# Kernel optimization log

Hardware: AMD Instinct MI355X
Metric: run time of the kernel (lower is better)

## Reference

```python
import jax, jax.numpy as jnp
import numpy as np

B, T, D, F, E = 4, 8192, 1024, 4096, 8


def setup_inputs() -> dict:
    key = jax.random.key(0)
    ks = jax.random.split(key, 5)
    s = 0.02
    return {
        "X": jax.random.normal(ks[0], (B, T, D), dtype=jnp.float32),
        "slots_w": jax.random.normal(ks[1], (E, D), dtype=jnp.float32) * s,
        "w1": jax.random.normal(ks[2], (E, F, D), dtype=jnp.float32) * s,
        "w3": jax.random.normal(ks[3], (E, F, D), dtype=jnp.float32) * s,
        "w2": jax.random.normal(ks[4], (E, D, F), dtype=jnp.float32) * s,
    }


def reference(X, slots_w, w1, w3, w2):
    # logits: [B,T,E]
    logits = jnp.einsum("btd,ed->bte", X, slots_w)
    dispatch_w = jax.nn.softmax(logits, axis=1)  # softmax over tokens
    combine_w = jax.nn.softmax(logits, axis=2)   # softmax over experts
    # slots: one D-vector per expert per batch -> [B,E,D]
    slots = jnp.einsum("bte,btd->bed", dispatch_w, X)
    # SwiGLU FFN batched over experts
    h = jax.nn.silu(jnp.einsum("bed,efd->bef", slots, w1)) * jnp.einsum("bed,efd->bef", slots, w3)
    y = jnp.einsum("bef,edf->bed", h, w2)  # [B,E,D]
    # combine back to tokens: [B,T,D]
    return jnp.einsum("bte,bed->btd", combine_w, y)
```

## Files before the change

### kernel.cpp

```cpp
#include <hip/hip_runtime.h>
#include <math.h>

#define NB 4
#define NT 8192
#define ND 1024
#define NF 4096
#define NE 8

#define K3_CHUNKS 128
#define K3_TPC (NT / K3_CHUNKS)
#define K7_CHB 256
#define K7_TOK (NT / K7_CHB)

typedef float v4f __attribute__((ext_vector_type(4)));

__device__ __forceinline__ float4 ntload4(const float* p) {
  v4f v = __builtin_nontemporal_load((const v4f*)p);
  return make_float4(v.x, v.y, v.z, v.w);
}
__device__ __forceinline__ void ntstore4(float* p, float4 a) {
  v4f v = {a.x, a.y, a.z, a.w};
  __builtin_nontemporal_store(v, (v4f*)p);
}

__device__ __forceinline__ float dot4(float4 a, float4 b) {
  return a.x * b.x + a.y * b.y + a.z * b.z + a.w * b.w;
}

__device__ __forceinline__ float reduce8(float v0, float v1, float v2, float v3,
                                         float v4, float v5, float v6, float v7,
                                         int lane) {
  const bool b0 = lane & 1;
  float s, u0, u1, u2, u3;
  s = b0 ? v0 : v1; u0 = (b0 ? v1 : v0) + __shfl_xor(s, 1);
  s = b0 ? v2 : v3; u1 = (b0 ? v3 : v2) + __shfl_xor(s, 1);
  s = b0 ? v4 : v5; u2 = (b0 ? v5 : v4) + __shfl_xor(s, 1);
  s = b0 ? v6 : v7; u3 = (b0 ? v7 : v6) + __shfl_xor(s, 1);
  const bool b1 = lane & 2;
  float w0, w1;
  s = b1 ? u0 : u1; w0 = (b1 ? u1 : u0) + __shfl_xor(s, 2);
  s = b1 ? u2 : u3; w1 = (b1 ? u3 : u2) + __shfl_xor(s, 2);
  const bool b2 = lane & 4;
  s = b2 ? w0 : w1; float x = (b2 ? w1 : w0) + __shfl_xor(s, 4);
  x += __shfl_xor(x, 8);
  x += __shfl_xor(x, 16);
  x += __shfl_xor(x, 32);
  return x;
}

__global__ __launch_bounds__(256, 4) void k_logits(const float* __restrict__ X,
                                                   const float* __restrict__ sw,
                                                   float* __restrict__ logits) {
  __shared__ float4 s_sw[NE * ND / 4];
  for (int i = threadIdx.x; i < NE * ND / 4; i += 256)
    s_sw[i] = ((const float4*)sw)[i];
  __syncthreads();
  const int lane = threadIdx.x & 63;
  const int wave = threadIdx.x >> 6;
  const int b = blockIdx.x >> 9;
  const int t0 = (blockIdx.x & 511) * 16;

  float4 Xc[4], Xn[4];
  {
    const float4* xr = (const float4*)(X + ((size_t)b * NT + t0 + wave) * ND);
#pragma unroll
    for (int it = 0; it < 4; ++it) Xc[it] = xr[it * 64 + lane];
  }
#pragma unroll
  for (int i = 0; i < 4; ++i) {
    const int t = t0 + wave + i * 4;
    if (i < 3) {
      const float4* xr = (const float4*)(X + ((size_t)b * NT + t + 4) * ND);
#pragma unroll
      for (int it = 0; it < 4; ++it) Xn[it] = xr[it * 64 + lane];
    }
    float acc[NE];
#pragma unroll
    for (int e = 0; e < NE; ++e) acc[e] = 0.f;
#pragma unroll
    for (int it = 0; it < 4; ++it) {
      float4 x = Xc[it];
#pragma unroll
      for (int e = 0; e < NE; ++e)
        acc[e] += dot4(x, s_sw[e * 256 + it * 64 + lane]);
    }
    float r = reduce8(acc[0], acc[1], acc[2], acc[3],
                      acc[4], acc[5], acc[6], acc[7], lane);
    if (lane < 8) logits[((size_t)b * NT + t) * NE + lane] = r;
#pragma unroll
    for (int it = 0; it < 4; ++it) Xc[it] = Xn[it];
  }
}

__global__ __launch_bounds__(256) void k_colstats(const float* __restrict__ logits,
                                                  float* __restrict__ M,
                                                  float* __restrict__ L) {
  const int b = blockIdx.x / NE;
  const int e = blockIdx.x % NE;
  const int tid = threadIdx.x;
  const int lane = tid & 63, wave = tid >> 6;
  const float* base = logits + (size_t)b * NT * NE + e;
  float v[NT / 256];
#pragma unroll
  for (int i = 0; i < NT / 256; ++i) v[i] = base[(size_t)(tid + i * 256) * NE];
  float mx = -1e30f;
#pragma unroll
  for (int i = 0; i < NT / 256; ++i) mx = fmaxf(mx, v[i]);
#pragma unroll
  for (int off = 32; off > 0; off >>= 1) mx = fmaxf(mx, __shfl_xor(mx, off));
  __shared__ float red[4];
  if (lane == 0) red[wave] = mx;
  __syncthreads();
  mx = fmaxf(fmaxf(red[0], red[1]), fmaxf(red[2], red[3]));
  float s = 0.f;
#pragma unroll
  for (int i = 0; i < NT / 256; ++i) s += expf(v[i] - mx);
#pragma unroll
  for (int off = 32; off > 0; off >>= 1) s += __shfl_xor(s, off);
  __syncthreads();
  if (lane == 0) red[wave] = s;
  __syncthreads();
  if (tid == 0) {
    M[blockIdx.x] = mx;
    L[blockIdx.x] = red[0] + red[1] + red[2] + red[3];
  }
}

__global__ __launch_bounds__(256, 2) void k_slots_partial(const float* __restrict__ X,
                                                          const float* __restrict__ logits,
                                                          const float* __restrict__ M,
                                                          float* __restrict__ partial) {
  __shared__ float pw[K3_TPC][NE];
  __shared__ float sM[NE];
  const int tid = threadIdx.x;
  const int b = blockIdx.x / K3_CHUNKS;
  const int chunk = blockIdx.x % K3_CHUNKS;
  const int t0 = chunk * K3_TPC;
  if (tid < NE) sM[tid] = M[b * NE + tid];
  __syncthreads();
  for (int i = tid; i < K3_TPC * NE; i += 256) {
    const int t = i >> 3, e = i & 7;
    pw[t][e] = expf(logits[((size_t)b * NT + t0 + t) * NE + e] - sM[e]);
  }
  __syncthreads();

  const float* xb = X + ((size_t)b * NT + t0) * ND + tid * 4;
  float4 Xc[8], Xn[8];
#pragma unroll
  for (int k = 0; k < 8; ++k) Xc[k] = *(const float4*)(xb + (size_t)k * ND);
  float4 acc[NE];
#pragma unroll
  for (int e = 0; e < NE; ++e) acc[e] = make_float4(0.f, 0.f, 0.f, 0.f);

  for (int g = 0; g < 8; ++g) {
    if (g < 7) {
#pragma unroll
      for (int k = 0; k < 8; ++k)
        Xn[k] = *(const float4*)(xb + (size_t)((g + 1) * 8 + k) * ND);
    }
#pragma unroll
    for (int k = 0; k < 8; ++k) {
      const int t = g * 8 + k;
      float4 pa = *(const float4*)&pw[t][0];
      float4 pb = *(const float4*)&pw[t][4];
      float4 x = Xc[k];
      acc[0].x += pa.x * x.x; acc[0].y += pa.x * x.y; acc[0].z += pa.x * x.z; acc[0].w += pa.x * x.w;
      acc[1].x += pa.y * x.x; acc[1].y += pa.y * x.y; acc[1].z += pa.y * x.z; acc[1].w += pa.y * x.w;
      acc[2].x += pa.z * x.x; acc[2].y += pa.z * x.y; acc[2].z += pa.z * x.z; acc[2].w += pa.z * x.w;
      acc[3].x += pa.w * x.x; acc[3].y += pa.w * x.y; acc[3].z += pa.w * x.z; acc[3].w += pa.w * x.w;
      acc[4].x += pb.x * x.x; acc[4].y += pb.x * x.y; acc[4].z += pb.x * x.z; acc[4].w += pb.x * x.w;
      acc[5].x += pb.y * x.x; acc[5].y += pb.y * x.y; acc[5].z += pb.y * x.z; acc[5].w += pb.y * x.w;
      acc[6].x += pb.z * x.x; acc[6].y += pb.z * x.y; acc[6].z += pb.z * x.z; acc[6].w += pb.z * x.w;
      acc[7].x += pb.w * x.x; acc[7].y += pb.w * x.y; acc[7].z += pb.w * x.z; acc[7].w += pb.w * x.w;
    }
#pragma unroll
    for (int k = 0; k < 8; ++k) Xc[k] = Xn[k];
  }
  float* pout = partial + (size_t)blockIdx.x * (NE * ND) + tid * 4;
#pragma unroll
  for (int e = 0; e < NE; ++e) *(float4*)(pout + e * ND) = acc[e];
}

__global__ __launch_bounds__(256, 4) void k_slots_reduce(const float* __restrict__ partial,
                                                         const float* __restrict__ L,
                                                         float* __restrict__ slots) {
  __shared__ float red[256];
  const int tid = threadIdx.x;
  const int half = tid >> 7;
  const int l128 = tid & 127;
  const int col = blockIdx.x * 128 + l128;
  const int b = col >> 13;
  const int ed = col & 8191;
  const float* p = partial + ((size_t)b * K3_CHUNKS + half * 64) * (NE * ND) + ed;
  float s = 0.f;
  for (int c = 0; c < 64; c += 8) {
#pragma unroll
    for (int k = 0; k < 8; ++k) s += p[(size_t)(c + k) * NE * ND];
  }
  red[tid] = s;
  __syncthreads();
  if (half == 0) {
    const int e = ed >> 10;
    slots[col] = (red[tid] + red[tid + 128]) / L[b * NE + e];
  }
}

__global__ __launch_bounds__(256, 4) void k_ffn1(const float* __restrict__ slots,
                                                 const float* __restrict__ w1,
                                                 const float* __restrict__ w3,
                                                 float* __restrict__ h) {
  __shared__ float4 s_sl[NB][ND / 4];
  const int tid = threadIdx.x;
  const int lane = tid & 63, wave = tid >> 6;
  const int e = blockIdx.x >> 8;
  const int f0 = (blockIdx.x & 255) * 16;
  for (int i = tid; i < NB * ND / 4; i += 256) {
    const int b = i >> 8, j = i & 255;
    s_sl[b][j] = ((const float4*)(slots + ((size_t)b * NE + e) * ND))[j];
  }
  __syncthreads();

  const float* w1e = w1 + (size_t)e * NF * ND;
  const float* w3e = w3 + (size_t)e * NF * ND;
  float4 W1c[4], W3c[4], W1n[4], W3n[4];
  {
    const int f = f0 + wave;
    const float* r1 = w1e + (size_t)f * ND;
    const float* r3 = w3e + (size_t)f * ND;
#pragma unroll
    for (int it = 0; it < 4; ++it) {
      W1c[it] = ntload4(r1 + (it * 64 + lane) * 4);
      W3c[it] = ntload4(r3 + (it * 64 + lane) * 4);
    }
  }
#pragma unroll
  for (int rg = 0; rg < 4; ++rg) {
    const int f = f0 + wave + rg * 4;
    if (rg < 3) {
      const float* r1 = w1e + (size_t)(f + 4) * ND;
      const float* r3 = w3e + (size_t)(f + 4) * ND;
#pragma unroll
      for (int it = 0; it < 4; ++it) {
        W1n[it] = ntload4(r1 + (it * 64 + lane) * 4);
        W3n[it] = ntload4(r3 + (it * 64 + lane) * 4);
      }
    }
    float a1[NB] = {0.f, 0.f, 0.f, 0.f}, a3[NB] = {0.f, 0.f, 0.f, 0.f};
#pragma unroll
    for (int it = 0; it < 4; ++it) {
      float4 x1 = W1c[it], x3 = W3c[it];
#pragma unroll
      for (int b = 0; b < NB; ++b) {
        float4 s = s_sl[b][it * 64 + lane];
        a1[b] += dot4(x1, s);
        a3[b] += dot4(x3, s);
      }
    }
    float x = reduce8(a1[0], a1[1], a1[2], a1[3],
                      a3[0], a3[1], a3[2], a3[3], lane);
    float other = __shfl_xor(x, 4);
    if (lane < 4) {
      const float sil = x / (1.f + expf(-x));
      h[((size_t)e * NB + lane) * NF + f] = sil * other;
    }
#pragma unroll
    for (int it = 0; it < 4; ++it) { W1c[it] = W1n[it]; W3c[it] = W3n[it]; }
  }
}

__global__ __launch_bounds__(256, 4) void k_ffn2(const float* __restrict__ h,
                                                 const float* __restrict__ w2,
                                                 float* __restrict__ y_part) {
  const int tid = threadIdx.x;
  const int lane = tid & 63, wave = tid >> 6;
  const int e = blockIdx.x >> 8;
  const int rem = blockIdx.x & 255;
  const int d0 = (rem >> 2) * 16;
  const int c = rem & 3;
  const int fb = c * 1024;

  const float* he = h + (size_t)e * NB * NF;
  const float* w2e = w2 + (size_t)e * ND * NF;
  const int r0 = d0 + wave * 4;

  float4 Wc[4], Wn[4], Hc[4], Hn[4];
  {
    const int pos = fb + lane * 4;
#pragma unroll
    for (int r = 0; r < 4; ++r) Wc[r] = ntload4(w2e + (size_t)(r0 + r) * NF + pos);
#pragma unroll
    for (int b = 0; b < NB; ++b) Hc[b] = *(const float4*)(he + (size_t)b * NF + pos);
  }
  float acc[4][NB];
#pragma unroll
  for (int r = 0; r < 4; ++r)
#pragma unroll
    for (int b = 0; b < NB; ++b) acc[r][b] = 0.f;

#pragma unroll
  for (int si = 0; si < 4; ++si) {
    if (si < 3) {
      const int pos = fb + (si + 1) * 256 + lane * 4;
#pragma unroll
      for (int r = 0; r < 4; ++r) Wn[r] = ntload4(w2e + (size_t)(r0 + r) * NF + pos);
#pragma unroll
      for (int b = 0; b < NB; ++b) Hn[b] = *(const float4*)(he + (size_t)b * NF + pos);
    }
#pragma unroll
    for (int r = 0; r < 4; ++r)
#pragma unroll
      for (int b = 0; b < NB; ++b) acc[r][b] += dot4(Wc[r], Hc[b]);
#pragma unroll
    for (int r = 0; r < 4; ++r) Wc[r] = Wn[r];
#pragma unroll
    for (int b = 0; b < NB; ++b) Hc[b] = Hn[b];
  }

  float x01 = reduce8(acc[0][0], acc[0][1], acc[0][2], acc[0][3],
                      acc[1][0], acc[1][1], acc[1][2], acc[1][3], lane);
  float x23 = reduce8(acc[2][0], acc[2][1], acc[2][2], acc[2][3],
                      acc[3][0], acc[3][1], acc[3][2], acc[3][3], lane);
  if (lane < 8) {
    const int b = lane & 3, r = lane >> 2;
    y_part[(((size_t)c * NB + b) * NE + e) * ND + r0 + r] = x01;
    y_part[(((size_t)c * NB + b) * NE + e) * ND + r0 + 2 + r] = x23;
  }
}

__global__ __launch_bounds__(256, 4) void k_combine(const float* __restrict__ logits,
                                                    const float* __restrict__ y_part,
                                                    float* __restrict__ out) {
  const int b = blockIdx.x >> 8;
  const int t0 = (blockIdx.x & 255) * K7_TOK;
  __shared__ float4 s_y[NE * ND / 4];
  const float4* yp = (const float4*)y_part;
  for (int i = threadIdx.x; i < NE * ND / 4; i += 256) {
    float4 a = yp[(size_t)(0 * NB + b) * 2048 + i];
    float4 c1 = yp[(size_t)(1 * NB + b) * 2048 + i];
    float4 c2 = yp[(size_t)(2 * NB + b) * 2048 + i];
    float4 c3 = yp[(size_t)(3 * NB + b) * 2048 + i];
    a.x += c1.x + c2.x + c3.x; a.y += c1.y + c2.y + c3.y;
    a.z += c1.z + c2.z + c3.z; a.w += c1.w + c2.w + c3.w;
    s_y[i] = a;
  }
  __shared__ float s_cw[K7_TOK][NE];
  if (threadIdx.x < K7_TOK) {
    const int t = t0 + threadIdx.x;
    const float* lg = logits + ((size_t)b * NT + t) * NE;
    float l[NE];
    float mx = -1e30f;
#pragma unroll
    for (int e = 0; e < NE; ++e) { l[e] = lg[e]; mx = fmaxf(mx, l[e]); }
    float s = 0.f;
#pragma unroll
    for (int e = 0; e < NE; ++e) { l[e] = expf(l[e] - mx); s += l[e]; }
    const float inv = 1.f / s;
#pragma unroll
    for (int e = 0; e < NE; ++e) s_cw[threadIdx.x][e] = l[e] * inv;
  }
  __syncthreads();
  for (int t = 0; t < K7_TOK; ++t) {
    float4 o = make_float4(0.f, 0.f, 0.f, 0.f);
#pragma unroll
    for (int e = 0; e < NE; ++e) {
      const float cw = s_cw[t][e];
      float4 yv = s_y[e * 256 + threadIdx.x];
      o.x += cw * yv.x; o.y += cw * yv.y; o.z += cw * yv.z; o.w += cw * yv.w;
    }
    ntstore4(out + ((size_t)b * NT + t0 + t) * ND + threadIdx.x * 4, o);
  }
}

extern "C" void kernel_launch(void* const* d_in, const int* in_sizes, int n_in,
                              void* d_out, int out_size, void* d_ws, size_t ws_size,
                              hipStream_t stream) {
  const float* X  = (const float*)d_in[0];
  const float* sw = (const float*)d_in[1];
  const float* w1 = (const float*)d_in[2];
  const float* w3 = (const float*)d_in[3];
  const float* w2 = (const float*)d_in[4];
  float* out = (float*)d_out;

  float* ws = (float*)d_ws;
  float* logits  = ws;
  float* M       = logits + (size_t)NB * NT * NE;
  float* L       = M + NB * NE;
  float* partial = L + NB * NE;
  float* slots   = partial + (size_t)NB * K3_CHUNKS * NE * ND;
  float* h       = slots + NB * NE * ND;
  float* y_part  = h + (size_t)NE * NB * NF;

  hipLaunchKernelGGL(k_logits, dim3(NB * (NT / 16)), dim3(256), 0, stream, X, sw, logits);
  hipLaunchKernelGGL(k_colstats, dim3(NB * NE), dim3(256), 0, stream, logits, M, L);
  hipLaunchKernelGGL(k_slots_partial, dim3(NB * K3_CHUNKS), dim3(256), 0, stream,
                     X, logits, M, partial);
  hipLaunchKernelGGL(k_slots_reduce, dim3(NB * NE * ND / 128), dim3(256), 0, stream,
                     partial, L, slots);
  hipLaunchKernelGGL(k_ffn1, dim3(NE * (NF / 16)), dim3(256), 0, stream, slots, w1, w3, h);
  hipLaunchKernelGGL(k_ffn2, dim3(NE * (ND / 16) * 4), dim3(256), 0, stream, h, w2, y_part);
  hipLaunchKernelGGL(k_combine, dim3(NB * K7_CHB), dim3(256), 0, stream, logits, y_part, out);
}
```

Before: 184.4 us.

## Fuse logits, column softmax stats and slot accumulation into one dispatch kernel

Merges the logits, column-stats and slot-partial kernels into one kernel. It computes each token's expert logits on the fly from register-resident router weights, exponentiates them, and accumulates both the weighted X partial sums and per-chunk softmax denominators in a single pass. This is meant to remove the second full read of X and two kernel launches. The token-softmax max subtraction is dropped and the denominator is instead summed from per-chunk partials in the reduce kernel, which risks overflow for large logits. It also adds three block barriers per token group, and raises k_ffn1's occupancy hint.

```diff
diff --git a/kernel.cpp b/kernel.cpp
--- a/kernel.cpp
+++ b/kernel.cpp
@@ -7,8 +7,8 @@
 #define NF 4096
 #define NE 8
 
-#define K3_CHUNKS 128
-#define K3_TPC (NT / K3_CHUNKS)
+#define DCH 128
+#define DTOK 64
 #define K7_CHB 256
 #define K7_TOK (NT / K7_CHB)
 
@@ -48,121 +48,69 @@
   return x;
 }
 
-__global__ __launch_bounds__(256, 4) void k_logits(const float* __restrict__ X,
-                                                   const float* __restrict__ sw,
-                                                   float* __restrict__ logits) {
-  __shared__ float4 s_sw[NE * ND / 4];
-  for (int i = threadIdx.x; i < NE * ND / 4; i += 256)
-    s_sw[i] = ((const float4*)sw)[i];
-  __syncthreads();
-  const int lane = threadIdx.x & 63;
-  const int wave = threadIdx.x >> 6;
-  const int b = blockIdx.x >> 9;
-  const int t0 = (blockIdx.x & 511) * 16;
-
-  float4 Xc[4], Xn[4];
-  {
-    const float4* xr = (const float4*)(X + ((size_t)b * NT + t0 + wave) * ND);
-#pragma unroll
-    for (int it = 0; it < 4; ++it) Xc[it] = xr[it * 64 + lane];
-  }
-#pragma unroll
-  for (int i = 0; i < 4; ++i) {
-    const int t = t0 + wave + i * 4;
-    if (i < 3) {
-      const float4* xr = (const float4*)(X + ((size_t)b * NT + t + 4) * ND);
-#pragma unroll
-      for (int it = 0; it < 4; ++it) Xn[it] = xr[it * 64 + lane];
-    }
-    float acc[NE];
-#pragma unroll
-    for (int e = 0; e < NE; ++e) acc[e] = 0.f;
-#pragma unroll
-    for (int it = 0; it < 4; ++it) {
-      float4 x = Xc[it];
-#pragma unroll
-      for (int e = 0; e < NE; ++e)
-        acc[e] += dot4(x, s_sw[e * 256 + it * 64 + lane]);
-    }
-    float r = reduce8(acc[0], acc[1], acc[2], acc[3],
-                      acc[4], acc[5], acc[6], acc[7], lane);
-    if (lane < 8) logits[((size_t)b * NT + t) * NE + lane] = r;
-#pragma unroll
-    for (int it = 0; it < 4; ++it) Xc[it] = Xn[it];
-  }
-}
-
-__global__ __launch_bounds__(256) void k_colstats(const float* __restrict__ logits,
-                                                  float* __restrict__ M,
-                                                  float* __restrict__ L) {
-  const int b = blockIdx.x / NE;
-  const int e = blockIdx.x % NE;
+__global__ __launch_bounds__(256, 2) void k_dispatch(const float* __restrict__ X,
+                                                     const float* __restrict__ sw,
+                                                     float* __restrict__ logits,
+                                                     float* __restrict__ partial,
+                                                     float* __restrict__ Lpart) {
   const int tid = threadIdx.x;
   const int lane = tid & 63, wave = tid >> 6;
-  const float* base = logits + (size_t)b * NT * NE + e;
-  float v[NT / 256];
-#pragma unroll
-  for (int i = 0; i < NT / 256; ++i) v[i] = base[(size_t)(tid + i * 256) * NE];
-  float mx = -1e30f;
-#pragma unroll
-  for (int i = 0; i < NT / 256; ++i) mx = fmaxf(mx, v[i]);
-#pragma unroll
-  for (int off = 32; off > 0; off >>= 1) mx = fmaxf(mx, __shfl_xor(mx, off));
-  __shared__ float red[4];
-  if (lane == 0) red[wave] = mx;
-  __syncthreads();
-  mx = fmaxf(fmaxf(red[0], red[1]), fmaxf(red[2], red[3]));
-  float s = 0.f;
-#pragma unroll
-  for (int i = 0; i < NT / 256; ++i) s += expf(v[i] - mx);
-#pragma unroll
-  for (int off = 32; off > 0; off >>= 1) s += __shfl_xor(s, off);
-  __syncthreads();
-  if (lane == 0) red[wave] = s;
-  __syncthreads();
-  if (tid == 0) {
-    M[blockIdx.x] = mx;
-    L[blockIdx.x] = red[0] + red[1] + red[2] + red[3];
-  }
-}
-
-__global__ __launch_bounds__(256, 2) void k_slots_partial(const float* __restrict__ X,
-                                                          const float* __restrict__ logits,
-                                                          const float* __restrict__ M,
-                                                          float* __restrict__ partial) {
-  __shared__ float pw[K3_TPC][NE];
-  __shared__ float sM[NE];
-  const int tid = threadIdx.x;
-  const int b = blockIdx.x / K3_CHUNKS;
-  const int chunk = blockIdx.x % K3_CHUNKS;
-  const int t0 = chunk * K3_TPC;
-  if (tid < NE) sM[tid] = M[b * NE + tid];
-  __syncthreads();
-  for (int i = tid; i < K3_TPC * NE; i += 256) {
-    const int t = i >> 3, e = i & 7;
-    pw[t][e] = expf(logits[((size_t)b * NT + t0 + t) * NE + e] - sM[e]);
-  }
-  __syncthreads();
+  const int b = blockIdx.x >> 7;
+  const int chunk = blockIdx.x & 127;
+  const int t0 = chunk * DTOK;
+
+  float4 swr[NE];
+#pragma unroll
+  for (int e = 0; e < NE; ++e)
+    swr[e] = *(const float4*)(sw + (size_t)e * ND + tid * 4);
+
+  __shared__ float wred[4][8][8];
+  __shared__ float pwt[8][8];
+  __shared__ float lsum[8][8];
 
   const float* xb = X + ((size_t)b * NT + t0) * ND + tid * 4;
   float4 Xc[8], Xn[8];
 #pragma unroll
-  for (int k = 0; k < 8; ++k) Xc[k] = *(const float4*)(xb + (size_t)k * ND);
+  for (int k = 0; k < 8; ++k) Xc[k] = ntload4(xb + (size_t)k * ND);
+
   float4 acc[NE];
 #pragma unroll
   for (int e = 0; e < NE; ++e) acc[e] = make_float4(0.f, 0.f, 0.f, 0.f);
+  float Lacc = 0.f;
 
   for (int g = 0; g < 8; ++g) {
     if (g < 7) {
 #pragma unroll
       for (int k = 0; k < 8; ++k)
-        Xn[k] = *(const float4*)(xb + (size_t)((g + 1) * 8 + k) * ND);
+        Xn[k] = ntload4(xb + (size_t)((g + 1) * 8 + k) * ND);
     }
 #pragma unroll
     for (int k = 0; k < 8; ++k) {
-      const int t = g * 8 + k;
-      float4 pa = *(const float4*)&pw[t][0];
-      float4 pb = *(const float4*)&pw[t][4];
+      float p0 = dot4(Xc[k], swr[0]), p1 = dot4(Xc[k], swr[1]);
+      float p2 = dot4(Xc[k], swr[2]), p3 = dot4(Xc[k], swr[3]);
+      float p4 = dot4(Xc[k], swr[4]), p5 = dot4(Xc[k], swr[5]);
+      float p6 = dot4(Xc[k], swr[6]), p7 = dot4(Xc[k], swr[7]);
+      float r = reduce8(p0, p1, p2, p3, p4, p5, p6, p7, lane);
+      if (lane < 8) wred[wave][k][lane] = r;
+    }
+    asm volatile("s_waitcnt lgkmcnt(0)" ::: "memory");
+    __builtin_amdgcn_s_barrier();
+    if (wave == 0) {
+      const int t = lane >> 3, e = lane & 7;
+      if (lane < 64) {
+        float lg = wred[0][t][e] + wred[1][t][e] + wred[2][t][e] + wred[3][t][e];
+        logits[((size_t)b * NT + t0 + g * 8 + t) * NE + e] = lg;
+        float ex = expf(lg);
+        pwt[t][e] = ex;
+        Lacc += ex;
+      }
+    }
+    asm volatile("s_waitcnt lgkmcnt(0)" ::: "memory");
+    __builtin_amdgcn_s_barrier();
+#pragma unroll
+    for (int k = 0; k < 8; ++k) {
+      float4 pa = *(const float4*)&pwt[k][0];
+      float4 pb = *(const float4*)&pwt[k][4];
       float4 x = Xc[k];
       acc[0].x += pa.x * x.x; acc[0].y += pa.x * x.y; acc[0].z += pa.x * x.z; acc[0].w += pa.x * x.w;
       acc[1].x += pa.y * x.x; acc[1].y += pa.y * x.y; acc[1].z += pa.y * x.z; acc[1].w += pa.y * x.w;
@@ -173,39 +121,45 @@
       acc[6].x += pb.z * x.x; acc[6].y += pb.z * x.y; acc[6].z += pb.z * x.z; acc[6].w += pb.z * x.w;
       acc[7].x += pb.w * x.x; acc[7].y += pb.w * x.y; acc[7].z += pb.w * x.z; acc[7].w += pb.w * x.w;
     }
+    asm volatile("s_waitcnt lgkmcnt(0)" ::: "memory");
+    __builtin_amdgcn_s_barrier();
 #pragma unroll
     for (int k = 0; k < 8; ++k) Xc[k] = Xn[k];
   }
+
   float* pout = partial + (size_t)blockIdx.x * (NE * ND) + tid * 4;
 #pragma unroll
   for (int e = 0; e < NE; ++e) *(float4*)(pout + e * ND) = acc[e];
+
+  if (wave == 0 && lane < 64) lsum[lane >> 3][lane & 7] = Lacc;
+  __syncthreads();
+  if (tid < 8) {
+    float s = 0.f;
+#pragma unroll
+    for (int t = 0; t < 8; ++t) s += lsum[t][tid];
+    Lpart[(size_t)blockIdx.x * NE + tid] = s;
+  }
 }
 
 __global__ __launch_bounds__(256, 4) void k_slots_reduce(const float* __restrict__ partial,
-                                                         const float* __restrict__ L,
+                                                         const float* __restrict__ Lpart,
                                                          float* __restrict__ slots) {
-  __shared__ float red[256];
-  const int tid = threadIdx.x;
-  const int half = tid >> 7;
-  const int l128 = tid & 127;
-  const int col = blockIdx.x * 128 + l128;
+  const int col = blockIdx.x * 256 + threadIdx.x;
   const int b = col >> 13;
   const int ed = col & 8191;
-  const float* p = partial + ((size_t)b * K3_CHUNKS + half * 64) * (NE * ND) + ed;
+  const int e = ed >> 10;
+  const float* p = partial + (size_t)b * DCH * (NE * ND) + ed;
   float s = 0.f;
-  for (int c = 0; c < 64; c += 8) {
-#pragma unroll
-    for (int k = 0; k < 8; ++k) s += p[(size_t)(c + k) * NE * ND];
-  }
-  red[tid] = s;
-  __syncthreads();
-  if (half == 0) {
-    const int e = ed >> 10;
-    slots[col] = (red[tid] + red[tid + 128]) / L[b * NE + e];
-  }
-}
-
-__global__ __launch_bounds__(256, 4) void k_ffn1(const float* __restrict__ slots,
+#pragma unroll 8
+  for (int c = 0; c < DCH; ++c) s += p[(size_t)c * NE * ND];
+  const float* lp = Lpart + (size_t)b * DCH * NE + e;
+  float Ls = 0.f;
+#pragma unroll 8
+  for (int c = 0; c < DCH; ++c) Ls += lp[c * NE];
+  slots[col] = s / Ls;
+}
+
+__global__ __launch_bounds__(256, 8) void k_ffn1(const float* __restrict__ slots,
                                                  const float* __restrict__ w1,
                                                  const float* __restrict__ w3,
                                                  float* __restrict__ h) {
@@ -383,20 +337,18 @@
 
   float* ws = (float*)d_ws;
   float* logits  = ws;
-  float* M       = logits + (size_t)NB * NT * NE;
-  float* L       = M + NB * NE;
-  float* partial = L + NB * NE;
-  float* slots   = partial + (size_t)NB * K3_CHUNKS * NE * ND;
+  float* partial = logits + (size_t)NB * NT * NE;
+  float* Lpart   = partial + (size_t)NB * DCH * NE * ND;
+  float* slots   = Lpart + (size_t)NB * DCH * NE;
   float* h       = slots + NB * NE * ND;
   float* y_part  = h + (size_t)NE * NB * NF;
 
-  hipLaunchKernelGGL(k_logits, dim3(NB * (NT / 16)), dim3(256), 0, stream, X, sw, logits);
-  hipLaunchKernelGGL(k_colstats, dim3(NB * NE), dim3(256), 0, stream, logits, M, L);
-  hipLaunchKernelGGL(k_slots_partial, dim3(NB * K3_CHUNKS), dim3(256), 0, stream,
-                     X, logits, M, partial);
-  hipLaunchKernelGGL(k_slots_reduce, dim3(NB * NE * ND / 128), dim3(256), 0, stream,
-                     partial, L, slots);
-  hipLaunchKernelGGL(k_ffn1, dim3(NE * (NF / 16)), dim3(256), 0, stream, slots, w1, w3, h);
+  hipLaunchKernelGGL(k_dispatch, dim3(NB * DCH), dim3(256), 0, stream,
+                     X, sw, logits, partial, Lpart);
+  hipLaunchKernelGGL(k_slots_reduce, dim3(NB * NE * ND / 256), dim3(256), 0, stream,
+                     partial, Lpart, slots);
+  hipLaunchKernelGGL(k_ffn1, dim3(NE * (NF / 16)), dim3(256), 0, stream,
+                     slots, w1, w3, h);
   hipLaunchKernelGGL(k_ffn2, dim3(NE * (ND / 16) * 4), dim3(256), 0, stream, h, w2, y_part);
   hipLaunchKernelGGL(k_combine, dim3(NB * K7_CHB), dim3(256), 0, stream, logits, y_part, out);
 }
```

Result: faster. 167.7 us (-9.1%).
